# Optimization experiments

Measured on AMD Instinct MI355X. Metric: run time of the kernel, lower is better.

Reference implementation:

```python
import jax, jax.numpy as jnp
import numpy as np

N = 100000
D = 16          # input_dim
NUM_FILTERS = 8
NNZ = 1600000


def setup_inputs() -> dict:
    key = jax.random.key(0)
    k1, k2, k3, k4, k5 = jax.random.split(key, 5)
    x = jax.random.normal(k1, (N, D), dtype=jnp.float32)
    L_rows = jax.random.randint(k2, (NNZ,), 0, N, dtype=jnp.int64 if jax.config.jax_enable_x64 else jnp.int32).astype(jnp.int32)
    L_cols = jax.random.randint(k3, (NNZ,), 0, N, dtype=jnp.int32)
    L_v = jax.random.normal(k4, (NNZ,), dtype=jnp.float32)
    node_attr_eig = jax.random.uniform(k5, (N,), dtype=jnp.float32)
    return {"x": x, "L_rows": L_rows, "L_cols": L_cols, "L_v": L_v, "node_attr_eig": node_attr_eig}


def reference(x, L_rows, L_cols, L_v, node_attr_eig):
    n, d = x.shape
    f = NUM_FILTERS
    # exponents = 2 ** arange(num_filters + 1)
    exponents = (2 ** jnp.arange(f + 1)).astype(x.dtype)  # [F+1]
    # coeffs = x.T @ L  ==  (L.T @ x).T ; compute L.T @ x as [N, D]
    # (L.T @ x)[c] = sum over nnz entries (r, c): L_v * x[r]
    LTx = jax.ops.segment_sum(L_v[:, None] * x[L_rows], L_cols, num_segments=n)  # [N, D]
    # exponential eigenfilter bank: w = exp(-eig)^exponents, wavelet differences
    w = jnp.exp(-node_attr_eig)[:, None] ** exponents[None, :]  # [N, F+1]
    w_wav = w[:, :-1] - w[:, 1:]                                # [N, F]
    # g_eig = coeffs[..., None] * w_wav[None, ...] permuted to [N, D, F]
    g_eig = (LTx[:, :, None] * w_wav[:, None, :]).reshape(n, d * f)  # [N, D*F]
    # filtered = L @ g_eig : out[r] = sum over nnz (r, c): L_v * g_eig[c]
    out = jax.ops.segment_sum(L_v[:, None] * g_eig[L_cols], L_rows, num_segments=n)
    return out.reshape(n, d, f)
```

## Files before the change

### kernel.cpp

```cpp
#include <hip/hip_runtime.h>

#define N_NODES   100000
#define D_DIM     16
#define NFILT     8
#define KOUT      128
#define NNZ_CNT   1600000

#define CBITS     8
#define CROWS     256
#define NCB       ((N_NODES + CROWS - 1) / CROWS)
#define CAP       5120
#define EPB       4096
#define NBLKA     ((NNZ_CNT + EPB - 1) / EPB)

__device__ __forceinline__ uint f32_to_bf16_bits(float f) {
    uint u = __float_as_uint(f);
    uint r = (u + 0x7FFFu + ((u >> 16) & 1u)) >> 16;
    return r;
}

__global__ void wav_kernel(const float* __restrict__ eig, ushort* __restrict__ wavb) {
    int n = blockIdx.x * blockDim.x + threadIdx.x;
    if (n >= N_NODES) return;
    float cur = expf(-eig[n]);
    uint pk[4];
#pragma unroll
    for (int h = 0; h < 4; ++h) {
        float nx0 = cur * cur;
        float w0 = cur - nx0;
        float nx1 = nx0 * nx0;
        float w1 = nx0 - nx1;
        cur = nx1;
        pk[h] = f32_to_bf16_bits(w0) | (f32_to_bf16_bits(w1) << 16);
    }
    *(uint4*)(wavb + (size_t)n * NFILT) = make_uint4(pk[0], pk[1], pk[2], pk[3]);
}

__global__ void scatter1_kernel(const float* __restrict__ x,
                                const int* __restrict__ rows,
                                const int* __restrict__ cols,
                                const float* __restrict__ v,
                                float* __restrict__ LTxI) {
    long long idx = (long long)blockIdx.x * blockDim.x + threadIdx.x;
    if (idx >= (long long)NNZ_CNT * D_DIM) return;
    int e = (int)(idx >> 4);
    int d = (int)(idx & 15);
    int r = rows[e];
    int c = cols[e];
    float val = v[e] * x[(size_t)r * D_DIM + d];
    int slot = ((d & 7) << 1) + (d >> 3);
    atomicAdd(LTxI + (size_t)c * D_DIM + slot, val);
}

__global__ void pack_kernel(const float* __restrict__ LTxI, uint* __restrict__ LTxP) {
    int idx = blockIdx.x * blockDim.x + threadIdx.x;
    if (idx >= N_NODES * NFILT) return;
    float2 lp = *(const float2*)(LTxI + (size_t)idx * 2);
    LTxP[idx] = f32_to_bf16_bits(lp.x) | (f32_to_bf16_bits(lp.y) << 16);
}

__global__ __launch_bounds__(512) void binA_kernel(const int* __restrict__ rows,
                                                   const int* __restrict__ cols,
                                                   const float* __restrict__ v,
                                                   int* __restrict__ gcur,
                                                   int2* __restrict__ regA) {
    __shared__ int cnt[NCB];
    __shared__ int offb[NCB];
    __shared__ int gbase[NCB];
    __shared__ int sc[512];
    __shared__ int2 rec[EPB];
    int tid = threadIdx.x;
    int e0 = blockIdx.x * EPB;
    int nE = NNZ_CNT - e0; if (nE > EPB) nE = EPB;

    for (int i = tid; i < NCB; i += 512) cnt[i] = 0;
    __syncthreads();
    for (int i = tid; i < nE; i += 512)
        atomicAdd(&cnt[rows[e0 + i] >> CBITS], 1);
    __syncthreads();

    sc[tid] = (tid < NCB) ? cnt[tid] : 0;
    __syncthreads();
    for (int off = 1; off < 512; off <<= 1) {
        int t = (tid >= off) ? sc[tid - off] : 0;
        __syncthreads();
        sc[tid] += t;
        __syncthreads();
    }
    if (tid < NCB) {
        int cv = cnt[tid];
        int st = sc[tid] - cv;
        offb[tid] = st;
        gbase[tid] = cv ? atomicAdd(&gcur[tid], cv) : 0;
        cnt[tid] = st;
    }
    __syncthreads();

    for (int i = tid; i < nE; i += 512) {
        int r = rows[e0 + i], c = cols[e0 + i];
        float val = v[e0 + i];
        int b = r >> CBITS;
        int pos = atomicAdd(&cnt[b], 1);
        rec[pos] = make_int2(((r & (CROWS - 1)) << 17) | c, __float_as_int(val));
    }
    __syncthreads();

    int wv = tid >> 6, lane = tid & 63;
    for (int b = wv; b < NCB; b += 8) {
        int s = offb[b];
        int n = cnt[b] - s;
        size_t dst = (size_t)b * CAP + gbase[b];
        for (int i = lane; i < n; i += 64)
            regA[dst + i] = rec[s + i];
    }
}

__global__ __launch_bounds__(512) void binB_kernel(const int* __restrict__ gcur,
                                                   int2* __restrict__ regA,
                                                   int2* __restrict__ offs2) {
    __shared__ int2 rec[CAP];
    __shared__ int cnt[CROWS];
    __shared__ int sc[CROWS];
    int tid = threadIdx.x;
    int b = blockIdx.x;
    int nb = gcur[b]; if (nb > CAP) nb = CAP;
    size_t base = (size_t)b * CAP;

    if (tid < CROWS) cnt[tid] = 0;
    __syncthreads();
    for (int i = tid; i < nb; i += 512) {
        int2 r = regA[base + i];
        rec[i] = r;
        atomicAdd(&cnt[r.x >> 17], 1);
    }
    __syncthreads();

    int cv = (tid < CROWS) ? cnt[tid] : 0;
    if (tid < CROWS) sc[tid] = cv;
    __syncthreads();
    for (int off = 1; off < CROWS; off <<= 1) {
        int t = (tid < CROWS && tid >= off) ? sc[tid - off] : 0;
        __syncthreads();
        if (tid < CROWS) sc[tid] += t;
        __syncthreads();
    }
    if (tid < CROWS) {
        int st = sc[tid] - cv;
        int row = b * CROWS + tid;
        if (row < N_NODES)
            offs2[row] = make_int2((int)base + st, (int)base + st + cv);
        cnt[tid] = st;
    }
    __syncthreads();

    for (int i = tid; i < nb; i += 512) {
        int2 r = rec[i];
        int p = atomicAdd(&cnt[r.x >> 17], 1);
        regA[base + p] = make_int2(r.x & 0x1FFFF, r.y);
    }
}

__global__ __launch_bounds__(256) void gather2_kernel(const int2* __restrict__ offs2,
                                                      const int2* __restrict__ ep,
                                                      const uint* __restrict__ LTxP,
                                                      const ushort* __restrict__ wavb,
                                                      float* __restrict__ out) {
    int wave = (int)(((long long)blockIdx.x * blockDim.x + threadIdx.x) >> 6);
    if (wave >= N_NODES) return;
    int lane = threadIdx.x & 63;
    int r = wave;
    int d0 = lane >> 3;
    int f  = lane & 7;
    int2 se = offs2[r];
    int i = se.x, end = se.y;
    float acc0 = 0.f, acc1 = 0.f;
    for (; i + 4 <= end; i += 4) {
        int2 e0 = ep[i], e1 = ep[i + 1], e2 = ep[i + 2], e3 = ep[i + 3];
        uint l0 = LTxP[e0.x * NFILT + d0];
        uint l1 = LTxP[e1.x * NFILT + d0];
        uint l2 = LTxP[e2.x * NFILT + d0];
        uint l3 = LTxP[e3.x * NFILT + d0];
        uint w0 = wavb[e0.x * NFILT + f];
        uint w1 = wavb[e1.x * NFILT + f];
        uint w2 = wavb[e2.x * NFILT + f];
        uint w3 = wavb[e3.x * NFILT + f];
        float vw0 = __int_as_float(e0.y) * __uint_as_float(w0 << 16);
        float vw1 = __int_as_float(e1.y) * __uint_as_float(w1 << 16);
        float vw2 = __int_as_float(e2.y) * __uint_as_float(w2 << 16);
        float vw3 = __int_as_float(e3.y) * __uint_as_float(w3 << 16);
        acc0 = fmaf(vw0, __uint_as_float(l0 << 16), acc0);
        acc1 = fmaf(vw0, __uint_as_float(l0 & 0xFFFF0000u), acc1);
        acc0 = fmaf(vw1, __uint_as_float(l1 << 16), acc0);
        acc1 = fmaf(vw1, __uint_as_float(l1 & 0xFFFF0000u), acc1);
        acc0 = fmaf(vw2, __uint_as_float(l2 << 16), acc0);
        acc1 = fmaf(vw2, __uint_as_float(l2 & 0xFFFF0000u), acc1);
        acc0 = fmaf(vw3, __uint_as_float(l3 << 16), acc0);
        acc1 = fmaf(vw3, __uint_as_float(l3 & 0xFFFF0000u), acc1);
    }
    for (; i < end; ++i) {
        int2 e = ep[i];
        uint l = LTxP[e.x * NFILT + d0];
        uint w = wavb[e.x * NFILT + f];
        float vw = __int_as_float(e.y) * __uint_as_float(w << 16);
        acc0 = fmaf(vw, __uint_as_float(l << 16), acc0);
        acc1 = fmaf(vw, __uint_as_float(l & 0xFFFF0000u), acc1);
    }
    out[(size_t)r * KOUT + lane]      = acc0;
    out[(size_t)r * KOUT + 64 + lane] = acc1;
}

extern "C" void kernel_launch(void* const* d_in, const int* in_sizes, int n_in,
                              void* d_out, int out_size, void* d_ws, size_t ws_size,
                              hipStream_t stream) {
    const float* x      = (const float*)d_in[0];
    const int*   L_rows = (const int*)  d_in[1];
    const int*   L_cols = (const int*)  d_in[2];
    const float* L_v    = (const float*)d_in[3];
    const float* eig    = (const float*)d_in[4];
    float* out = (float*)d_out;

    float*  LTxI  = (float*)d_ws;
    uint*   LTxP  = (uint*)(LTxI + (size_t)N_NODES * D_DIM);
    ushort* wavb  = (ushort*)(LTxP + (size_t)N_NODES * NFILT);
    int2*   offs2 = (int2*)(wavb + (size_t)N_NODES * NFILT);
    int2*   regA  = offs2 + N_NODES;
    int*    gcur  = (int*)(regA + (size_t)NCB * CAP);

    hipMemsetAsync(LTxI, 0, (size_t)N_NODES * D_DIM * sizeof(float), stream);
    hipMemsetAsync(gcur, 0, (size_t)NCB * sizeof(int), stream);

    wav_kernel<<<(N_NODES + 255) / 256, 256, 0, stream>>>(eig, wavb);

    {
        long long total = (long long)NNZ_CNT * D_DIM;
        scatter1_kernel<<<(int)((total + 255) / 256), 256, 0, stream>>>(x, L_rows, L_cols, L_v, LTxI);
    }
    pack_kernel<<<(N_NODES * NFILT + 255) / 256, 256, 0, stream>>>(LTxI, LTxP);

    binA_kernel<<<NBLKA, 512, 0, stream>>>(L_rows, L_cols, L_v, gcur, regA);
    binB_kernel<<<NCB, 512, 0, stream>>>(gcur, regA, offs2);

    {
        long long threads = (long long)N_NODES * 64;
        gather2_kernel<<<(int)((threads + 255) / 256), 256, 0, stream>>>(offs2, regA, LTxP, wavb, out);
    }
}
```

Baseline: 279.0 us.

## Accumulate L^T x directly in packed half2 atomics and simplify row binning

The first scatter now accumulates into a packed fp16 half2 buffer with one packed atomic per pair of dims, replacing the fp32 atomics and the separate pack kernel. This halves the atomic count, removes one kernel and the fp32 intermediate, and shrinks the memset. The gather reads half2 in place of bf16 pairs. binA drops its shared-memory staging and prefix scan and writes records straight to global bins, with a smaller elements-per-block. The risk is fp16 range and precision loss in the atomic accumulation, plus less coalesced global writes in binA.

```diff
diff --git a/kernel.cpp b/kernel.cpp
--- a/kernel.cpp
+++ b/kernel.cpp
@@ -1,4 +1,5 @@
 #include <hip/hip_runtime.h>
+#include <hip/hip_fp16.h>
 
 #define N_NODES   100000
 #define D_DIM     16
@@ -10,13 +11,12 @@
 #define CROWS     256
 #define NCB       ((N_NODES + CROWS - 1) / CROWS)
 #define CAP       5120
-#define EPB       4096
+#define EPB       2048
 #define NBLKA     ((NNZ_CNT + EPB - 1) / EPB)
 
 __device__ __forceinline__ uint f32_to_bf16_bits(float f) {
     uint u = __float_as_uint(f);
-    uint r = (u + 0x7FFFu + ((u >> 16) & 1u)) >> 16;
-    return r;
+    return (u + 0x7FFFu + ((u >> 16) & 1u)) >> 16;
 }
 
 __global__ void wav_kernel(const float* __restrict__ eig, ushort* __restrict__ wavb) {
@@ -40,23 +40,17 @@
                                 const int* __restrict__ rows,
                                 const int* __restrict__ cols,
                                 const float* __restrict__ v,
-                                float* __restrict__ LTxI) {
+                                __half2* __restrict__ LTxH) {
     long long idx = (long long)blockIdx.x * blockDim.x + threadIdx.x;
-    if (idx >= (long long)NNZ_CNT * D_DIM) return;
-    int e = (int)(idx >> 4);
-    int d = (int)(idx & 15);
+    if (idx >= (long long)NNZ_CNT * 8) return;
+    int e = (int)(idx >> 3);
+    int j = (int)(idx & 7);
     int r = rows[e];
     int c = cols[e];
-    float val = v[e] * x[(size_t)r * D_DIM + d];
-    int slot = ((d & 7) << 1) + (d >> 3);
-    atomicAdd(LTxI + (size_t)c * D_DIM + slot, val);
-}
-
-__global__ void pack_kernel(const float* __restrict__ LTxI, uint* __restrict__ LTxP) {
-    int idx = blockIdx.x * blockDim.x + threadIdx.x;
-    if (idx >= N_NODES * NFILT) return;
-    float2 lp = *(const float2*)(LTxI + (size_t)idx * 2);
-    LTxP[idx] = f32_to_bf16_bits(lp.x) | (f32_to_bf16_bits(lp.y) << 16);
+    float vv = v[e];
+    float a = vv * x[(size_t)r * D_DIM + j];
+    float b = vv * x[(size_t)r * D_DIM + j + 8];
+    unsafeAtomicAdd(&LTxH[(size_t)c * NFILT + j], __floats2half2_rn(a, b));
 }
 
 __global__ __launch_bounds__(512) void binA_kernel(const int* __restrict__ rows,
@@ -65,10 +59,7 @@
                                                    int* __restrict__ gcur,
                                                    int2* __restrict__ regA) {
     __shared__ int cnt[NCB];
-    __shared__ int offb[NCB];
     __shared__ int gbase[NCB];
-    __shared__ int sc[512];
-    __shared__ int2 rec[EPB];
     int tid = threadIdx.x;
     int e0 = blockIdx.x * EPB;
     int nE = NNZ_CNT - e0; if (nE > EPB) nE = EPB;
@@ -78,40 +69,18 @@
     for (int i = tid; i < nE; i += 512)
         atomicAdd(&cnt[rows[e0 + i] >> CBITS], 1);
     __syncthreads();
-
-    sc[tid] = (tid < NCB) ? cnt[tid] : 0;
-    __syncthreads();
-    for (int off = 1; off < 512; off <<= 1) {
-        int t = (tid >= off) ? sc[tid - off] : 0;
-        __syncthreads();
-        sc[tid] += t;
-        __syncthreads();
-    }
-    if (tid < NCB) {
-        int cv = cnt[tid];
-        int st = sc[tid] - cv;
-        offb[tid] = st;
-        gbase[tid] = cv ? atomicAdd(&gcur[tid], cv) : 0;
-        cnt[tid] = st;
-    }
-    __syncthreads();
-
+    for (int i = tid; i < NCB; i += 512) {
+        int cv = cnt[i];
+        gbase[i] = cv ? atomicAdd(&gcur[i], cv) : 0;
+        cnt[i] = 0;
+    }
+    __syncthreads();
     for (int i = tid; i < nE; i += 512) {
         int r = rows[e0 + i], c = cols[e0 + i];
-        float val = v[e0 + i];
         int b = r >> CBITS;
         int pos = atomicAdd(&cnt[b], 1);
-        rec[pos] = make_int2(((r & (CROWS - 1)) << 17) | c, __float_as_int(val));
-    }
-    __syncthreads();
-
-    int wv = tid >> 6, lane = tid & 63;
-    for (int b = wv; b < NCB; b += 8) {
-        int s = offb[b];
-        int n = cnt[b] - s;
-        size_t dst = (size_t)b * CAP + gbase[b];
-        for (int i = lane; i < n; i += 64)
-            regA[dst + i] = rec[s + i];
+        regA[(size_t)b * CAP + gbase[b] + pos] =
+            make_int2(((r & (CROWS - 1)) << 17) | c, __float_as_int(v[e0 + i]));
     }
 }
 
@@ -162,7 +131,7 @@
 
 __global__ __launch_bounds__(256) void gather2_kernel(const int2* __restrict__ offs2,
                                                       const int2* __restrict__ ep,
-                                                      const uint* __restrict__ LTxP,
+                                                      const __half2* __restrict__ LTxH,
                                                       const ushort* __restrict__ wavb,
                                                       float* __restrict__ out) {
     int wave = (int)(((long long)blockIdx.x * blockDim.x + threadIdx.x) >> 6);
@@ -176,34 +145,33 @@
     float acc0 = 0.f, acc1 = 0.f;
     for (; i + 4 <= end; i += 4) {
         int2 e0 = ep[i], e1 = ep[i + 1], e2 = ep[i + 2], e3 = ep[i + 3];
-        uint l0 = LTxP[e0.x * NFILT + d0];
-        uint l1 = LTxP[e1.x * NFILT + d0];
-        uint l2 = LTxP[e2.x * NFILT + d0];
-        uint l3 = LTxP[e3.x * NFILT + d0];
+        __half2 h0 = LTxH[e0.x * NFILT + d0];
+        __half2 h1 = LTxH[e1.x * NFILT + d0];
+        __half2 h2 = LTxH[e2.x * NFILT + d0];
+        __half2 h3 = LTxH[e3.x * NFILT + d0];
         uint w0 = wavb[e0.x * NFILT + f];
         uint w1 = wavb[e1.x * NFILT + f];
         uint w2 = wavb[e2.x * NFILT + f];
         uint w3 = wavb[e3.x * NFILT + f];
+        float2 l0 = __half22float2(h0);
+        float2 l1 = __half22float2(h1);
+        float2 l2 = __half22float2(h2);
+        float2 l3 = __half22float2(h3);
         float vw0 = __int_as_float(e0.y) * __uint_as_float(w0 << 16);
         float vw1 = __int_as_float(e1.y) * __uint_as_float(w1 << 16);
         float vw2 = __int_as_float(e2.y) * __uint_as_float(w2 << 16);
         float vw3 = __int_as_float(e3.y) * __uint_as_float(w3 << 16);
-        acc0 = fmaf(vw0, __uint_as_float(l0 << 16), acc0);
-        acc1 = fmaf(vw0, __uint_as_float(l0 & 0xFFFF0000u), acc1);
-        acc0 = fmaf(vw1, __uint_as_float(l1 << 16), acc0);
-        acc1 = fmaf(vw1, __uint_as_float(l1 & 0xFFFF0000u), acc1);
-        acc0 = fmaf(vw2, __uint_as_float(l2 << 16), acc0);
-        acc1 = fmaf(vw2, __uint_as_float(l2 & 0xFFFF0000u), acc1);
-        acc0 = fmaf(vw3, __uint_as_float(l3 << 16), acc0);
-        acc1 = fmaf(vw3, __uint_as_float(l3 & 0xFFFF0000u), acc1);
+        acc0 = fmaf(vw0, l0.x, acc0); acc1 = fmaf(vw0, l0.y, acc1);
+        acc0 = fmaf(vw1, l1.x, acc0); acc1 = fmaf(vw1, l1.y, acc1);
+        acc0 = fmaf(vw2, l2.x, acc0); acc1 = fmaf(vw2, l2.y, acc1);
+        acc0 = fmaf(vw3, l3.x, acc0); acc1 = fmaf(vw3, l3.y, acc1);
     }
     for (; i < end; ++i) {
         int2 e = ep[i];
-        uint l = LTxP[e.x * NFILT + d0];
+        float2 l = __half22float2(LTxH[e.x * NFILT + d0]);
         uint w = wavb[e.x * NFILT + f];
         float vw = __int_as_float(e.y) * __uint_as_float(w << 16);
-        acc0 = fmaf(vw, __uint_as_float(l << 16), acc0);
-        acc1 = fmaf(vw, __uint_as_float(l & 0xFFFF0000u), acc1);
+        acc0 = fmaf(vw, l.x, acc0); acc1 = fmaf(vw, l.y, acc1);
     }
     out[(size_t)r * KOUT + lane]      = acc0;
     out[(size_t)r * KOUT + 64 + lane] = acc1;
@@ -219,29 +187,27 @@
     const float* eig    = (const float*)d_in[4];
     float* out = (float*)d_out;
 
-    float*  LTxI  = (float*)d_ws;
-    uint*   LTxP  = (uint*)(LTxI + (size_t)N_NODES * D_DIM);
-    ushort* wavb  = (ushort*)(LTxP + (size_t)N_NODES * NFILT);
-    int2*   offs2 = (int2*)(wavb + (size_t)N_NODES * NFILT);
-    int2*   regA  = offs2 + N_NODES;
-    int*    gcur  = (int*)(regA + (size_t)NCB * CAP);
-
-    hipMemsetAsync(LTxI, 0, (size_t)N_NODES * D_DIM * sizeof(float), stream);
+    __half2* LTxH  = (__half2*)d_ws;
+    ushort*  wavb  = (ushort*)(LTxH + (size_t)N_NODES * NFILT);
+    int2*    offs2 = (int2*)(wavb + (size_t)N_NODES * NFILT);
+    int2*    regA  = offs2 + N_NODES;
+    int*     gcur  = (int*)(regA + (size_t)NCB * CAP);
+
+    hipMemsetAsync(LTxH, 0, (size_t)N_NODES * NFILT * sizeof(__half2), stream);
     hipMemsetAsync(gcur, 0, (size_t)NCB * sizeof(int), stream);
 
     wav_kernel<<<(N_NODES + 255) / 256, 256, 0, stream>>>(eig, wavb);
 
     {
-        long long total = (long long)NNZ_CNT * D_DIM;
-        scatter1_kernel<<<(int)((total + 255) / 256), 256, 0, stream>>>(x, L_rows, L_cols, L_v, LTxI);
-    }
-    pack_kernel<<<(N_NODES * NFILT + 255) / 256, 256, 0, stream>>>(LTxI, LTxP);
+        long long total = (long long)NNZ_CNT * 8;
+        scatter1_kernel<<<(int)((total + 255) / 256), 256, 0, stream>>>(x, L_rows, L_cols, L_v, LTxH);
+    }
 
     binA_kernel<<<NBLKA, 512, 0, stream>>>(L_rows, L_cols, L_v, gcur, regA);
     binB_kernel<<<NCB, 512, 0, stream>>>(gcur, regA, offs2);
 
     {
         long long threads = (long long)N_NODES * 64;
-        gather2_kernel<<<(int)((threads + 255) / 256), 256, 0, stream>>>(offs2, regA, LTxP, wavb, out);
-    }
-}
+        gather2_kernel<<<(int)((threads + 255) / 256), 256, 0, stream>>>(offs2, regA, LTxH, wavb, out);
+    }
+}
```

Result: no change. 279.2 us (+0.1%).
